# Performance work log

Hardware: AMD Instinct MI355X
Metric: run time of the kernel (lower is better)

The kernel has to match this reference:

```python
import jax, jax.numpy as jnp
import numpy as np


def setup_inputs() -> dict:
    key = jax.random.key(0)
    ks = jax.random.split(key, 7)
    B, T, C, D = 8, 2048, 1024, 128
    x = jax.random.normal(ks[0], (B, T, C), dtype=jnp.float32)
    # torch nn.Linear weights are [out_features, in_features]
    s = 1.0 / np.sqrt(C)
    Wq = jax.random.normal(ks[1], (D, C), dtype=jnp.float32) * s
    bq = jax.random.normal(ks[2], (D,), dtype=jnp.float32) * s
    Wk = jax.random.normal(ks[3], (D, C), dtype=jnp.float32) * s
    bk = jax.random.normal(ks[4], (D,), dtype=jnp.float32) * s
    Wv = jax.random.normal(ks[5], (D, C), dtype=jnp.float32) * s
    bv = jax.random.normal(ks[6], (D,), dtype=jnp.float32) * s
    return {"x": x, "Wq": Wq, "bq": bq, "Wk": Wk, "bk": bk, "Wv": Wv, "bv": bv}


def reference(x, Wq, bq, Wk, bk, Wv, bv):
    B, T, C = x.shape
    q = jnp.einsum('btc,dc->btd', x, Wq) + bq  # [B,T,D]
    k = jnp.einsum('btc,dc->btd', x, Wk) + bk
    v = jnp.einsum('btc,dc->btd', x, Wv) + bv
    scores = jnp.einsum('btd,bsd->bts', q, k)  # [B,T,T]
    causal = jnp.tril(jnp.ones((T, T), dtype=bool))
    masked = jnp.where(causal, scores, -jnp.inf)
    # NOTE: original scales by sqrt(key.weight.shape[-1]) == sqrt(emb_dim), AFTER masking
    scale = jnp.asarray(C, dtype=x.dtype) ** 0.5
    attn = jax.nn.softmax(masked / scale, axis=-1)
    return jnp.einsum('bts,bsd->btd', attn, v)
```

## Files before the change

kernel.cpp:

```cpp
#include <hip/hip_runtime.h>
#include <hip/hip_bf16.h>
#include <math.h>

typedef __bf16 bf16_t;
typedef __bf16 bf16x4 __attribute__((ext_vector_type(4)));
typedef __bf16 bf16x8 __attribute__((ext_vector_type(8)));
typedef float  f32x4  __attribute__((ext_vector_type(4)));
typedef float  f32x16 __attribute__((ext_vector_type(16)));
typedef int    v2i    __attribute__((ext_vector_type(2)));

static constexpr int Bz = 8, Tt = 2048, Cc = 1024, Dd = 128;
static constexpr int Mm = Bz * Tt;
static constexpr int NT128 = Tt / 128;

__device__ __forceinline__ bf16x8 lds_read8(const char* base, int byte) {
    return *(const bf16x8*)(base + byte);
}

__device__ __forceinline__ bf16x8 cvt8(float4 a, float4 b) {
    bf16x8 r;
    r[0] = (bf16_t)a.x; r[1] = (bf16_t)a.y; r[2] = (bf16_t)a.z; r[3] = (bf16_t)a.w;
    r[4] = (bf16_t)b.x; r[5] = (bf16_t)b.y; r[6] = (bf16_t)b.z; r[7] = (bf16_t)b.w;
    return r;
}

__device__ __forceinline__ unsigned cvtpk(float lo, float hi) {
    unsigned r;
    asm("v_cvt_pk_bf16_f32 %0, %1, %2" : "=v"(r) : "v"(lo), "v"(hi));
    return r;
}

typedef const __attribute__((address_space(1))) unsigned int* as1_u32p;
typedef __attribute__((address_space(3))) unsigned int* as3_u32p;

__device__ __forceinline__ void gload_lds16(const bf16_t* g, bf16_t* l) {
    __builtin_amdgcn_global_load_lds((as1_u32p)(const void*)g, (as3_u32p)(void*)l, 16, 0, 0);
}

__global__ __launch_bounds__(256) void wcvt_kernel(
    const float* __restrict__ Wq, const float* __restrict__ Wk,
    const float* __restrict__ Wv, bf16_t* __restrict__ Wp)
{
    int g = (blockIdx.x * 256 + threadIdx.x) * 4;
    int n = g >> 10;
    int k = g & 1023;
    int sel = n >> 7;
    const float* W = (sel == 0) ? Wq : (sel == 1) ? Wk : Wv;
    float4 f = *(const float4*)(W + (size_t)(n & 127) * 1024 + k);
    bf16x4 o; o[0] = (bf16_t)f.x; o[1] = (bf16_t)f.y; o[2] = (bf16_t)f.z; o[3] = (bf16_t)f.w;
    int ktile = k >> 6, kk = (k >> 5) & 1, hi = (k >> 3) & 3, e = k & 7;
    int ng = n >> 4, cg = ng / 12, ngl = ng % 12, lo = n & 15;
    size_t addr = (size_t)(((((ktile * 2 + cg) * 12 + ngl) * 2 + kk) * 4 + hi) * 16 + lo) * 8 + e;
    *(bf16x4*)(Wp + addr) = o;
}

__global__ __launch_bounds__(512, 4) void qkv_fused(
    const float* __restrict__ x, const bf16_t* __restrict__ Wp,
    const float* __restrict__ bq, const float* __restrict__ bk, const float* __restrict__ bv,
    bf16_t* __restrict__ qo, bf16_t* __restrict__ ko, bf16_t* __restrict__ vTo)
{
    const int m0  = blockIdx.x * 64;
    const int cg  = blockIdx.y;
    const int tid = threadIdx.x;
    const int lane = tid & 63;
    const int wv  = tid >> 6;
    const int wr  = wv >> 2;
    const int cw  = wv & 3;
    const int lo  = lane & 15;
    const int hi  = lane >> 4;

    __shared__ bf16_t Wl[2][12 * 2 * 512];
    __shared__ bf16_t Xs[2][64 * 64];

    f32x4 zero4 = {0.f, 0.f, 0.f, 0.f};
    f32x4 acc[2][3];
    #pragma unroll
    for (int i = 0; i < 2; i++)
        #pragma unroll
        for (int j = 0; j < 3; j++) acc[i][j] = zero4;

    const int xrow = tid >> 3;
    const int xcol = (tid & 7) * 8;

    float4 fx[2];
    auto load_x = [&](int t) {
        const float4* s = (const float4*)(x + (size_t)(m0 + xrow) * Cc + t * 64 + xcol);
        fx[0] = s[0]; fx[1] = s[1];
    };
    auto write_x = [&](int buf) {
        int byte = (xrow * 128 + xcol * 2) ^ ((xrow & 7) << 4);
        *(bf16x8*)((char*)Xs[buf] + byte) = cvt8(fx[0], fx[1]);
    };
    auto stage_W = [&](int buf, int t) {
        const bf16_t* base = Wp + (size_t)(t * 2 + cg) * 12288;
        #pragma unroll
        for (int i = 0; i < 3; i++) {
            int c = i * 8 + wv;
            gload_lds16(base + c * 512 + lane * 8, Wl[buf] + c * 512);
        }
    };
    auto compute = [&](int buf) {
        #pragma unroll
        for (int kk = 0; kk < 2; kk++) {
            int r0 = wr * 32 + lo;
            int r1 = wr * 32 + 16 + lo;
            bf16x8 af0 = lds_read8((char*)Xs[buf], (r0 * 128 + kk * 64 + hi * 16) ^ ((r0 & 7) << 4));
            bf16x8 af1 = lds_read8((char*)Xs[buf], (r1 * 128 + kk * 64 + hi * 16) ^ ((r1 & 7) << 4));
            #pragma unroll
            for (int j = 0; j < 3; j++) {
                bf16x8 bf = *(const bf16x8*)(Wl[buf] + ((cw * 3 + j) * 2 + kk) * 512 + lane * 8);
                acc[0][j] = __builtin_amdgcn_mfma_f32_16x16x32_bf16(af0, bf, acc[0][j], 0, 0, 0);
                acc[1][j] = __builtin_amdgcn_mfma_f32_16x16x32_bf16(af1, bf, acc[1][j], 0, 0, 0);
            }
        }
    };

    load_x(0);
    stage_W(0, 0);
    write_x(0);
    asm volatile("s_waitcnt lgkmcnt(0)" ::: "memory");
    __builtin_amdgcn_s_barrier();

    #pragma unroll 1
    for (int t = 0; t < 16; t++) {
        const int buf = t & 1;
        if (t < 15) {
            load_x(t + 1);
            stage_W(buf ^ 1, t + 1);
            asm volatile("s_waitcnt vmcnt(5)" ::: "memory");
        } else {
            asm volatile("s_waitcnt vmcnt(0)" ::: "memory");
        }
        __builtin_amdgcn_sched_barrier(0);
        compute(buf);
        if (t < 15) {
            write_x(buf ^ 1);
            asm volatile("s_waitcnt lgkmcnt(0)" ::: "memory");
            __builtin_amdgcn_s_barrier();
        }
    }

    #pragma unroll
    for (int j = 0; j < 3; j++) {
        int n = cg * 192 + cw * 48 + j * 16 + lo;
        int tsel = n >> 7, d = n & 127;
        const float* bp = (tsel == 0) ? bq : (tsel == 1) ? bk : bv;
        float bb = bp[d];
        #pragma unroll
        for (int i = 0; i < 2; i++)
            #pragma unroll
            for (int r = 0; r < 4; r++) {
                int m = m0 + wr * 32 + i * 16 + hi * 4 + r;
                float v = acc[i][j][r] + bb;
                if (tsel == 0)      qo[(size_t)m * Dd + d] = (bf16_t)v;
                else if (tsel == 1) ko[(size_t)m * Dd + d] = (bf16_t)v;
                else                vTo[(size_t)d * Mm + m] = (bf16_t)v;
            }
    }
}

__global__ __launch_bounds__(256, 2) void attn_kernel(
    const bf16_t* __restrict__ qi, const bf16_t* __restrict__ ki,
    const bf16_t* __restrict__ vTi,
    bf16_t* __restrict__ Opart, float* __restrict__ Mpart, float* __restrict__ Lpart,
    int nsplit)
{
    const int g   = blockIdx.x;
    const int per = nsplit * 8;
    const int qt  = (NT128 - 1) - g / per;
    const int rem = g % per;
    const int s   = rem >> 3;
    const int b   = rem & 7;
    const int nt  = 2 * qt + 2;
    const int t_lo = (s * nt) / nsplit;
    const int t_hi = ((s + 1) * nt) / nsplit;

    const int q0   = qt * 128;
    const int tid  = threadIdx.x;
    const int lane = tid & 63;
    const int w    = tid >> 6;
    const int rq   = lane & 31;
    const int dh   = lane >> 5;

    bf16_t* Ob = Opart + ((size_t)s * Mm + (size_t)b * Tt + q0) * Dd;
    float* Mb = Mpart + (size_t)s * Mm + (size_t)b * Tt + q0;
    float* Lb = Lpart + (size_t)s * Mm + (size_t)b * Tt + q0;

    if (t_lo >= t_hi) {
        float4 z = {0.f, 0.f, 0.f, 0.f};
        #pragma unroll
        for (int i = 0; i < 8; i++)
            ((float4*)Ob)[i * 256 + tid] = z;
        if (tid < 128) { Mb[tid] = -INFINITY; Lb[tid] = 0.f; }
        return;
    }

    __shared__ __align__(16) char smem[65536];

    const float SCALE = 1.4426950408889634f / 32.0f;
    const int qg = q0 + w * 32 + rq;
    const int qwmax = q0 + w * 32 + 31;

    bf16x8 qf[8];
    {
        const bf16_t* qrow = qi + (size_t)(b * Tt + qg) * Dd;
        #pragma unroll
        for (int ks = 0; ks < 8; ks++)
            qf[ks] = *(const bf16x8*)(qrow + ks * 16 + dh * 8);
    }

    f32x16 accO[4];
    #pragma unroll
    for (int ds = 0; ds < 4; ds++)
        #pragma unroll
        for (int e = 0; e < 16; e++) accO[ds][e] = 0.f;
    float mrun = -INFINITY, lrun = 0.f;

    const int krow = tid >> 2;
    const int kcol = (tid & 3) * 32;
    const int vrow = tid >> 1;
    const int vcol = (tid & 1) * 32;

    bf16x8 kr[4], vr[4];
    auto load_kv = [&](int t) {
        const int kv0 = t * 64;
        const bf16_t* ksrc = ki + (size_t)(b * Tt + kv0 + krow) * Dd + kcol;
        #pragma unroll
        for (int i = 0; i < 4; i++) kr[i] = *(const bf16x8*)(ksrc + i * 8);
        const bf16_t* vsrc = vTi + (size_t)vrow * Mm + (b * Tt + kv0 + vcol);
        #pragma unroll
        for (int i = 0; i < 4; i++) vr[i] = *(const bf16x8*)(vsrc + i * 8);
    };
    auto write_kv = [&](int buf) {
        char* Ksb = smem + buf * 16384;
        char* Vsb = smem + 32768 + buf * 16384;
        #pragma unroll
        for (int i = 0; i < 4; i++) {
            int byte = (krow * 256 + (kcol + i * 8) * 2) ^ ((krow & 15) << 4);
            *(bf16x8*)(Ksb + byte) = kr[i];
        }
        const int vlr = vrow & 63;
        const int vlc = (vrow >> 6) * 64 + vcol;
        #pragma unroll
        for (int i = 0; i < 4; i++) {
            int byte = (vlr * 256 + (vlc + i * 8) * 2) ^ ((vlr & 15) << 4);
            *(bf16x8*)(Vsb + byte) = vr[i];
        }
    };

    load_kv(t_lo);
    write_kv(0);
    int buf = 0;

    for (int t = t_lo; t < t_hi; t++) {
        const int kv0 = t * 64;
        const bool more = (t + 1 < t_hi);
        __syncthreads();
        if (more) load_kv(t + 1);

        if (kv0 <= qwmax) {
            const char* Ksb = smem + buf * 16384;
            const char* Vsb = smem + 32768 + buf * 16384;

            f32x16 accS0, accS1;
            #pragma unroll
            for (int e = 0; e < 16; e++) { accS0[e] = 0.f; accS1[e] = 0.f; }
            #pragma unroll
            for (int ks = 0; ks < 8; ks++) {
                int colb = (ks * 16 + dh * 8) * 2;
                bf16x8 kf0 = lds_read8(Ksb, ((rq)      * 256 + colb) ^ ((rq & 15) << 4));
                bf16x8 kf1 = lds_read8(Ksb, ((32 + rq) * 256 + colb) ^ ((rq & 15) << 4));
                accS0 = __builtin_amdgcn_mfma_f32_32x32x16_bf16(kf0, qf[ks], accS0, 0, 0, 0);
                accS1 = __builtin_amdgcn_mfma_f32_32x32x16_bf16(kf1, qf[ks], accS1, 0, 0, 0);
            }

            float pl[32];
            #pragma unroll
            for (int e = 0; e < 16; e++) {
                pl[e]      = accS0[e] * SCALE;
                pl[16 + e] = accS1[e] * SCALE;
            }
            if (kv0 + 63 > qg) {
                #pragma unroll
                for (int e = 0; e < 16; e++) {
                    int kg = kv0 + 8 * (e >> 2) + (e & 3) + 4 * dh;
                    if (kg > qg)      pl[e]      = -INFINITY;
                    if (kg + 32 > qg) pl[16 + e] = -INFINITY;
                }
            }

            float mt = pl[0];
            #pragma unroll
            for (int e = 1; e < 32; e++) mt = fmaxf(mt, pl[e]);
            mt = fmaxf(mt, __shfl_xor(mt, 32, 64));
            float mnew = fmaxf(mrun, mt);
            float muse = (mnew == -INFINITY) ? 0.f : mnew;
            float alpha = exp2f(mrun - muse);
            mrun = mnew;
            float ps = 0.f;
            #pragma unroll
            for (int e = 0; e < 32; e++) {
                float pv = exp2f(pl[e] - muse);
                pl[e] = pv;
                ps += pv;
            }
            lrun = alpha * lrun + ps;
            #pragma unroll
            for (int ds = 0; ds < 4; ds++)
                #pragma unroll
                for (int e = 0; e < 16; e++) accO[ds][e] *= alpha;

            unsigned u0[8], u1[8];
            #pragma unroll
            for (int gg = 0; gg < 8; gg++) {
                u0[gg] = cvtpk(pl[4 * gg + 0], pl[4 * gg + 1]);
                u1[gg] = cvtpk(pl[4 * gg + 2], pl[4 * gg + 3]);
            }
            bf16x8 pa[4];
            #pragma unroll
            for (int ks = 0; ks < 4; ks++) {
                v2i rA = __builtin_amdgcn_permlane32_swap((int)u0[2 * ks], (int)u0[2 * ks + 1], false, false);
                v2i rB = __builtin_amdgcn_permlane32_swap((int)u1[2 * ks], (int)u1[2 * ks + 1], false, false);
                union { unsigned wd[4]; bf16x8 v; } pu;
                pu.wd[0] = (unsigned)rA[0];
                pu.wd[1] = (unsigned)rB[0];
                pu.wd[2] = (unsigned)rA[1];
                pu.wd[3] = (unsigned)rB[1];
                pa[ks] = pu.v;
            }

            #pragma unroll
            for (int ds = 0; ds < 4; ds++) {
                int row  = (ds & 1) * 32 + rq;
                int cb   = (ds >> 1) * 64;
                #pragma unroll
                for (int ks = 0; ks < 4; ks++) {
                    int colb = (cb + ks * 16 + dh * 8) * 2;
                    bf16x8 vf = lds_read8(Vsb, (row * 256 + colb) ^ ((row & 15) << 4));
                    accO[ds] = __builtin_amdgcn_mfma_f32_32x32x16_bf16(vf, pa[ks], accO[ds], 0, 0, 0);
                }
            }
        }

        __syncthreads();
        if (more) write_kv(buf ^ 1);
        buf ^= 1;
    }

    __syncthreads();

    lrun += __shfl_xor(lrun, 32, 64);

    char* slab = smem + w * 8192;
    #pragma unroll
    for (int half = 0; half < 2; half++) {
        #pragma unroll
        for (int dsl = 0; dsl < 2; dsl++) {
            #pragma unroll
            for (int e = 0; e < 16; e++) {
                int d = 8 * (e >> 2) + (e & 3) + 4 * dh + 32 * dsl;
                int byte = (rq * 256 + d * 4) ^ ((rq & 15) << 4);
                *(float*)(slab + byte) = accO[half * 2 + dsl][e];
            }
        }
        __builtin_amdgcn_s_waitcnt(0);
        #pragma unroll
        for (int i = 0; i < 8; i++) {
            int dd = 32 * dh + 4 * i;
            int byte = (rq * 256 + dd * 4) ^ ((rq & 15) << 4);
            float4 val = *(float4*)(slab + byte);
            bf16x4 o; o[0] = (bf16_t)val.x; o[1] = (bf16_t)val.y;
            o[2] = (bf16_t)val.z; o[3] = (bf16_t)val.w;
            *(bf16x4*)(Ob + (size_t)(w * 32 + rq) * Dd + half * 64 + dd) = o;
        }
        __builtin_amdgcn_s_waitcnt(0);
    }

    if (lane < 32) {
        Mb[w * 32 + rq] = mrun;
        Lb[w * 32 + rq] = lrun;
    }
}

__global__ __launch_bounds__(256) void combine_kernel(
    const bf16_t* __restrict__ Opart, const float* __restrict__ Mpart,
    const float* __restrict__ Lpart, float* __restrict__ out, int nsplit)
{
    int t   = blockIdx.x * 256 + threadIdx.x;
    int row = t >> 5;
    int dq  = (t & 31) << 2;
    float M = -INFINITY;
    for (int s = 0; s < nsplit; s++)
        M = fmaxf(M, Mpart[(size_t)s * Mm + row]);
    float L = 0.f;
    float o0 = 0.f, o1 = 0.f, o2 = 0.f, o3 = 0.f;
    for (int s = 0; s < nsplit; s++) {
        float ms = Mpart[(size_t)s * Mm + row];
        float ws = (ms == -INFINITY) ? 0.f : exp2f(ms - M);
        L += ws * Lpart[(size_t)s * Mm + row];
        bf16x4 p = *(const bf16x4*)(Opart + ((size_t)s * Mm + row) * Dd + dq);
        o0 += ws * (float)p[0]; o1 += ws * (float)p[1];
        o2 += ws * (float)p[2]; o3 += ws * (float)p[3];
    }
    float inv = 1.0f / L;
    float4 r; r.x = o0 * inv; r.y = o1 * inv; r.z = o2 * inv; r.w = o3 * inv;
    *(float4*)(out + (size_t)row * Dd + dq) = r;
}

extern "C" void kernel_launch(void* const* d_in, const int* in_sizes, int n_in,
                              void* d_out, int out_size, void* d_ws, size_t ws_size,
                              hipStream_t stream)
{
    const float* x  = (const float*)d_in[0];
    const float* Wq = (const float*)d_in[1];
    const float* bq = (const float*)d_in[2];
    const float* Wk = (const float*)d_in[3];
    const float* bk = (const float*)d_in[4];
    const float* Wv = (const float*)d_in[5];
    const float* bv = (const float*)d_in[6];
    float* out = (float*)d_out;

    bf16_t* qb = (bf16_t*)d_ws;
    bf16_t* kb = qb + (size_t)Mm * Dd;
    bf16_t* vT = kb + (size_t)Mm * Dd;
    bf16_t* Wp = vT + (size_t)Mm * Dd;
    char* p = (char*)(Wp + (size_t)384 * Cc);

    auto need = [&](int ns) {
        return (size_t)3 * Mm * Dd * 2 + (size_t)384 * Cc * 2
             + (size_t)ns * Mm * Dd * 2 + (size_t)ns * Mm * 8;
    };
    int nsplit = 4;
    while (nsplit > 1 && need(nsplit) > ws_size) nsplit >>= 1;

    bf16_t* Opart = (bf16_t*)p;
    float* Mpart = (float*)(p + (size_t)nsplit * Mm * Dd * 2);
    float* Lpart = Mpart + (size_t)nsplit * Mm;

    wcvt_kernel<<<dim3(384), 256, 0, stream>>>(Wq, Wk, Wv, Wp);
    qkv_fused<<<dim3(256, 2), 512, 0, stream>>>(x, Wp, bq, bk, bv, qb, kb, vT);
    attn_kernel<<<dim3(NT128 * nsplit * Bz), 256, 0, stream>>>(qb, kb, vT, Opart, Mpart, Lpart, nsplit);
    combine_kernel<<<dim3(Mm * 32 / 256), 256, 0, stream>>>(Opart, Mpart, Lpart, out, nsplit);
}
```

Baseline: 65.70 us.

## Use per-query-tile variable split counts for balanced causal attention work

Replaces the uniform key-split count with a per-query-tile split count that grows with the causal length, so each block processes roughly the same number of key tiles. Blocks are mapped via constant prefix tables, and the empty-block path is removed. The combine kernel reads only the splits used for each row. This aims to reduce load imbalance and idle blocks, at the cost of more partial-result memory (sized for eight splits) without checking the workspace size.

Result: slower. 74.52 us (+13.4%).

```diff
diff --git a/kernel.cpp b/kernel.cpp
--- a/kernel.cpp
+++ b/kernel.cpp
@@ -12,6 +12,11 @@
 static constexpr int Bz = 8, Tt = 2048, Cc = 1024, Dd = 128;
 static constexpr int Mm = Bz * Tt;
 static constexpr int NT128 = Tt / 128;
+static constexpr int NSMAX = 8;
+static constexpr int NU = 72;
+
+__device__ __constant__ int SPL[16] = {1,1,2,2,3,3,4,4,5,5,6,6,7,7,8,8};
+__device__ __constant__ int PRE[16] = {0,1,2,4,6,9,12,16,20,25,30,36,42,49,56,64};
 
 __device__ __forceinline__ bf16x8 lds_read8(const char* base, int byte) {
     return *(const bf16x8*)(base + byte);
@@ -162,18 +167,20 @@
 __global__ __launch_bounds__(256, 2) void attn_kernel(
     const bf16_t* __restrict__ qi, const bf16_t* __restrict__ ki,
     const bf16_t* __restrict__ vTi,
-    bf16_t* __restrict__ Opart, float* __restrict__ Mpart, float* __restrict__ Lpart,
-    int nsplit)
+    bf16_t* __restrict__ Opart, float* __restrict__ Mpart, float* __restrict__ Lpart)
 {
-    const int g   = blockIdx.x;
-    const int per = nsplit * 8;
-    const int qt  = (NT128 - 1) - g / per;
-    const int rem = g % per;
-    const int s   = rem >> 3;
-    const int b   = rem & 7;
-    const int nt  = 2 * qt + 2;
-    const int t_lo = (s * nt) / nsplit;
-    const int t_hi = ((s + 1) * nt) / nsplit;
+    const int g  = blockIdx.x;
+    const int up = (NU - 1) - (g >> 3);
+    const int b  = g & 7;
+    int qt = 15;
+    #pragma unroll 1
+    for (int q = 0; q < 16; q++)
+        if (up >= PRE[q] && up < PRE[q] + SPL[q]) qt = q;
+    const int ns = SPL[qt];
+    const int s  = up - PRE[qt];
+    const int nt = 2 * qt + 2;
+    const int t_lo = (s * nt) / ns;
+    const int t_hi = ((s + 1) * nt) / ns;
 
     const int q0   = qt * 128;
     const int tid  = threadIdx.x;
@@ -185,15 +192,6 @@
     bf16_t* Ob = Opart + ((size_t)s * Mm + (size_t)b * Tt + q0) * Dd;
     float* Mb = Mpart + (size_t)s * Mm + (size_t)b * Tt + q0;
     float* Lb = Lpart + (size_t)s * Mm + (size_t)b * Tt + q0;
-
-    if (t_lo >= t_hi) {
-        float4 z = {0.f, 0.f, 0.f, 0.f};
-        #pragma unroll
-        for (int i = 0; i < 8; i++)
-            ((float4*)Ob)[i * 256 + tid] = z;
-        if (tid < 128) { Mb[tid] = -INFINITY; Lb[tid] = 0.f; }
-        return;
-    }
 
     __shared__ __align__(16) char smem[65536];
 
@@ -384,17 +382,19 @@
 
 __global__ __launch_bounds__(256) void combine_kernel(
     const bf16_t* __restrict__ Opart, const float* __restrict__ Mpart,
-    const float* __restrict__ Lpart, float* __restrict__ out, int nsplit)
+    const float* __restrict__ Lpart, float* __restrict__ out)
 {
     int t   = blockIdx.x * 256 + threadIdx.x;
     int row = t >> 5;
     int dq  = (t & 31) << 2;
+    int qt  = (row & (Tt - 1)) >> 7;
+    int ns  = SPL[qt];
     float M = -INFINITY;
-    for (int s = 0; s < nsplit; s++)
+    for (int s = 0; s < ns; s++)
         M = fmaxf(M, Mpart[(size_t)s * Mm + row]);
     float L = 0.f;
     float o0 = 0.f, o1 = 0.f, o2 = 0.f, o3 = 0.f;
-    for (int s = 0; s < nsplit; s++) {
+    for (int s = 0; s < ns; s++) {
         float ms = Mpart[(size_t)s * Mm + row];
         float ws = (ms == -INFINITY) ? 0.f : exp2f(ms - M);
         L += ws * Lpart[(size_t)s * Mm + row];
@@ -426,19 +426,12 @@
     bf16_t* Wp = vT + (size_t)Mm * Dd;
     char* p = (char*)(Wp + (size_t)384 * Cc);
 
-    auto need = [&](int ns) {
-        return (size_t)3 * Mm * Dd * 2 + (size_t)384 * Cc * 2
-             + (size_t)ns * Mm * Dd * 2 + (size_t)ns * Mm * 8;
-    };
-    int nsplit = 4;
-    while (nsplit > 1 && need(nsplit) > ws_size) nsplit >>= 1;
-
     bf16_t* Opart = (bf16_t*)p;
-    float* Mpart = (float*)(p + (size_t)nsplit * Mm * Dd * 2);
-    float* Lpart = Mpart + (size_t)nsplit * Mm;
+    float* Mpart = (float*)(p + (size_t)NSMAX * Mm * Dd * 2);
+    float* Lpart = Mpart + (size_t)NSMAX * Mm;
 
     wcvt_kernel<<<dim3(384), 256, 0, stream>>>(Wq, Wk, Wv, Wp);
     qkv_fused<<<dim3(256, 2), 512, 0, stream>>>(x, Wp, bq, bk, bv, qb, kb, vT);
-    attn_kernel<<<dim3(NT128 * nsplit * Bz), 256, 0, stream>>>(qb, kb, vT, Opart, Mpart, Lpart, nsplit);
-    combine_kernel<<<dim3(Mm * 32 / 256), 256, 0, stream>>>(Opart, Mpart, Lpart, out, nsplit);
-}
+    attn_kernel<<<dim3(NU * Bz), 256, 0, stream>>>(qb, kb, vT, Opart, Mpart, Lpart);
+    combine_kernel<<<dim3(Mm * 32 / 256), 256, 0, stream>>>(Opart, Mpart, Lpart, out);
+}
```
